# Kernel tuning notes

Measured on AMD Instinct MI355X. Metric: run time of the kernel, lower is better.

Reference implementation:

```python
import jax, jax.numpy as jnp
import numpy as np

GROUPS = 32
EPS = 1e-5


def _group_norm(x, scale, bias):
    B, C, H, W = x.shape
    xg = x.reshape(B, GROUPS, -1)
    mu = xg.mean(axis=-1, keepdims=True)
    var = jnp.mean(jnp.square(xg - mu), axis=-1, keepdims=True)
    xn = ((xg - mu) * jax.lax.rsqrt(var + EPS)).reshape(B, C, H, W)
    return xn * scale[None, :, None, None] + bias[None, :, None, None]


def _conv1x1(x, w, b):
    # x: [B,C,H,W], w: [O,C], b: [O]
    return jnp.einsum('bchw,oc->bohw', x, w) + b[None, :, None, None]


def setup_inputs() -> dict:
    key = jax.random.key(0)
    ks = jax.random.split(key, 6)
    B, C, H, W = 16, 512, 32, 32
    x = jax.random.normal(ks[0], (B, C, H, W), dtype=jnp.float32)
    # xavier_uniform for [C, C, 1, 1] conv: limit = sqrt(6 / (fan_in + fan_out)) = sqrt(6 / (2C))
    lim = float(np.sqrt(6.0 / (2 * C)))
    wq = jax.random.uniform(ks[1], (C, C), jnp.float32, -lim, lim)
    wk = jax.random.uniform(ks[2], (C, C), jnp.float32, -lim, lim)
    wv = jax.random.uniform(ks[3], (C, C), jnp.float32, -lim, lim)
    wo = jax.random.uniform(ks[4], (C, C), jnp.float32, -lim, lim) * 1e-5  # gain=1e-5
    zeros_c = jnp.zeros((C,), jnp.float32)
    return {
        'x': x,
        'gn_scale': jnp.ones((C,), jnp.float32),
        'gn_bias': zeros_c,
        'wq': wq, 'bq': zeros_c,
        'wk': wk, 'bk': zeros_c,
        'wv': wv, 'bv': zeros_c,
        'wo': wo, 'bo': zeros_c,
    }


def reference(x, gn_scale, gn_bias, wq, bq, wk, bk, wv, bv, wo, bo):
    B, C, H, W = x.shape
    N = H * W
    h = _group_norm(x, gn_scale, gn_bias)
    q = _conv1x1(h, wq, bq).reshape(B, C, N)  # [B,C,N]
    k = _conv1x1(h, wk, bk).reshape(B, C, N)
    v = _conv1x1(h, wv, bv).reshape(B, C, N)
    scale = 1.0 / jnp.sqrt(jnp.asarray(C, x.dtype))
    w = jnp.einsum('bcn,bcm->bnm', q, k) * scale  # [B,N,N]
    w = jax.nn.softmax(w, axis=-1)
    hv = jnp.einsum('bnm,bcm->bcn', w, v).reshape(B, C, H, W)
    out = _conv1x1(hv, wo, bo)
    return x + out
```

## Files before the change

kernel.cpp:

```cpp
#include <hip/hip_runtime.h>
#include <hip/hip_bf16.h>
#include <cstdint>

typedef unsigned char u8;
typedef float floatx4 __attribute__((ext_vector_type(4)));
typedef int intx8 __attribute__((ext_vector_type(8)));

__device__ __forceinline__ void gld_lds16(const void* g, void* l) {
    __builtin_amdgcn_global_load_lds(
        (const __attribute__((address_space(1))) unsigned int*)g,
        (__attribute__((address_space(3))) unsigned int*)l, 16, 0, 0);
}

__device__ __forceinline__ u8 f2fp8(float v) {
    return (u8)(__builtin_amdgcn_cvt_pk_fp8_f32(v, v, 0, false) & 0xff);
}
__device__ __forceinline__ unsigned int pack4_fp8(float a, float b, float c, float d) {
    unsigned int u = __builtin_amdgcn_cvt_pk_fp8_f32(a, b, 0, false);
    u = __builtin_amdgcn_cvt_pk_fp8_f32(c, d, u, true);
    return u;
}

__device__ __forceinline__ intx8 ld_frag(const u8* p, int lo, int hi) {
    uint4 a = *(const uint4*)(p + lo);
    uint4 b = *(const uint4*)(p + hi);
    intx8 r;
    r[0] = a.x; r[1] = a.y; r[2] = a.z; r[3] = a.w;
    r[4] = b.x; r[5] = b.y; r[6] = b.z; r[7] = b.w;
    return r;
}

__global__ __launch_bounds__(256) void setup_kernel(
    const float* __restrict__ x, const float* __restrict__ gs,
    const float* __restrict__ gb,
    const float* __restrict__ wq, const float* __restrict__ wk,
    const float* __restrict__ wv, const float* __restrict__ wo,
    const float* __restrict__ bq, const float* __restrict__ bk,
    const float* __restrict__ bv,
    u8* __restrict__ hT, u8* __restrict__ wqkv, u8* __restrict__ wob,
    float* __restrict__ bqkv, float* __restrict__ lsum)
{
    const int t = threadIdx.x;
    if (blockIdx.x >= 512) {
        int i = (blockIdx.x - 512) * 256 + t;
        if (i < 786432) {
            int which = i >> 18;
            int off = i & 262143;
            const float* src = which == 0 ? wq : which == 1 ? wk : wv;
            wqkv[i] = f2fp8(src[off]);
        } else {
            wob[i - 786432] = f2fp8(wo[i - 786432] * 262144.0f);
        }
        if (i < 1536)
            bqkv[i] = i < 512 ? bq[i] : (i < 1024 ? bk[i - 512] : bv[i - 1024]);
        if (i < 16384)
            lsum[i] = 0.0f;
        return;
    }
    const int b = blockIdx.x >> 5;
    const int g = blockIdx.x & 31;
    const int wave = t >> 6, lane = t & 63;
    const float4* x4 = (const float4*)(x + ((long long)b * 512 + g * 16) * 1024);

    float4 v[16];
    float s1 = 0.f, s2 = 0.f;
#pragma unroll
    for (int i = 0; i < 16; ++i) {
        v[i] = x4[i * 256 + t];
        s1 += v[i].x + v[i].y + v[i].z + v[i].w;
        s2 += v[i].x * v[i].x + v[i].y * v[i].y + v[i].z * v[i].z + v[i].w * v[i].w;
    }
#pragma unroll
    for (int m = 32; m; m >>= 1) {
        s1 += __shfl_xor(s1, m, 64);
        s2 += __shfl_xor(s2, m, 64);
    }
    __shared__ float red[2][4];
    __shared__ float stats[2];
    if (lane == 0) { red[0][wave] = s1; red[1][wave] = s2; }
    __syncthreads();
    if (t == 0) {
        float a = red[0][0] + red[0][1] + red[0][2] + red[0][3];
        float q = red[1][0] + red[1][1] + red[1][2] + red[1][3];
        float mu = a * (1.0f / 16384.0f);
        float var = q * (1.0f / 16384.0f) - mu * mu;
        stats[0] = mu;
        stats[1] = rsqrtf(var + 1e-5f);
    }
    __syncthreads();
    const float mu = stats[0], rs = stats[1];

#pragma unroll
    for (int i = 0; i < 16; ++i) {
        const float sc = gs[g * 16 + i] * rs;
        const float bi = gb[g * 16 + i] - mu * sc;
        v[i].x = v[i].x * sc + bi;
        v[i].y = v[i].y * sc + bi;
        v[i].z = v[i].z * sc + bi;
        v[i].w = v[i].w * sc + bi;
    }
    u8* hb = hT + (long long)b * 524288 + g * 16;
#pragma unroll
    for (int r = 0; r < 4; ++r) {
        uint4 o;
        o.x = pack4_fp8(v[0][r],  v[1][r],  v[2][r],  v[3][r]);
        o.y = pack4_fp8(v[4][r],  v[5][r],  v[6][r],  v[7][r]);
        o.z = pack4_fp8(v[8][r],  v[9][r],  v[10][r], v[11][r]);
        o.w = pack4_fp8(v[12][r], v[13][r], v[14][r], v[15][r]);
        *(uint4*)(hb + (long long)(4 * t + r) * 512) = o;
    }
}

template <int EPI>
__global__ __launch_bounds__(256, 3) void gemm_mx(
    const u8* __restrict__ A, long long sA,
    const u8* __restrict__ B, long long sB,
    void* __restrict__ C, long long sC,
    void* __restrict__ C2, void* __restrict__ C3,
    int ldC, int K,
    const float* __restrict__ bias,
    const float* __restrict__ resid, long long sR,
    float scale, float* __restrict__ lsum)
{
    __shared__ __align__(16) u8 smem[33792];
    const int tid = threadIdx.x;
    const int l = tid & 63;
    const int wave = tid >> 6;
    const int wm = wave >> 1, wn = wave & 1;
    const int bm = blockIdx.x, bn = blockIdx.y, b = blockIdx.z;

    const u8* Ab = A + (long long)b * sA + (long long)bm * 128 * K;
    const u8* Bb = B + (long long)b * sB + (long long)bn * 128 * K;

    const int srow = wave * 8 + (l >> 3);
    const int sg = ((l & 7) ^ ((l >> 3) & 7)) * 16;
    const u8* ga  = Ab + (long long)srow * K + sg;
    const u8* gbp = Bb + (long long)srow * K + sg;
    const long long c32 = (long long)32 * K;
    const int ldst = wave * 1024;

    const int q4 = l >> 4;
    const int glo = ((2 * q4) ^ (l & 7)) * 16;
    const int ghi = ((2 * q4 + 1) ^ (l & 7)) * 16;
    int arow[4], brow[4];
#pragma unroll
    for (int i = 0; i < 4; ++i) {
        arow[i] = (wm * 64 + i * 16 + (l & 15)) * 128;
        brow[i] = (wn * 64 + i * 16 + (l & 15)) * 128 + 16384;
    }

    floatx4 acc[4][4] = {};
    const int niter = K >> 7;

    for (int it = 0; it < niter; ++it) {
        const int k0 = it << 7;
#pragma unroll
        for (int c = 0; c < 4; ++c) {
            gld_lds16(ga + c * c32 + k0, smem + c * 4096 + ldst);
            gld_lds16(gbp + c * c32 + k0, smem + 16384 + c * 4096 + ldst);
        }
        __syncthreads();
        intx8 bfr[4];
#pragma unroll
        for (int j = 0; j < 4; ++j) bfr[j] = ld_frag(smem + brow[j], glo, ghi);
#pragma unroll
        for (int i = 0; i < 4; ++i) {
            intx8 af = ld_frag(smem + arow[i], glo, ghi);
#pragma unroll
            for (int j = 0; j < 4; ++j)
                acc[i][j] = __builtin_amdgcn_mfma_scale_f32_16x16x128_f8f6f4(
                    af, bfr[j], acc[i][j], 0, 0, 0, 127, 0, 127);
        }
        __syncthreads();
    }

    if (EPI == 3) {
        float* Cf = (float*)C;
#pragma unroll
        for (int i = 0; i < 4; ++i) {
            const int mrow = bm * 128 + wm * 64 + i * 16 + q4 * 4;
#pragma unroll
            for (int j = 0; j < 4; ++j) {
                const int ncol = bn * 128 + wn * 64 + j * 16 + (l & 15);
#pragma unroll
                for (int r = 0; r < 4; ++r) {
                    const int row = mrow + r;
                    float v = acc[i][j][r] * scale + bias[row] +
                              resid[(long long)b * sR + (long long)row * ldC + ncol];
                    Cf[(long long)b * sC + (long long)row * ldC + ncol] = v;
                }
            }
        }
    } else if (EPI == 1) {
        const int which = bn >> 2;
        u8* tile = smem;
#pragma unroll
        for (int i = 0; i < 4; ++i) {
            const int rl = wm * 64 + i * 16 + q4 * 4;
#pragma unroll
            for (int j = 0; j < 4; ++j) {
                const int cl = wn * 64 + j * 16 + (l & 15);
                const float badd = bias[bn * 128 + cl];
                if (which == 2) {
                    *(unsigned int*)(tile + cl * 144 + rl) =
                        pack4_fp8(acc[i][j][0] + badd, acc[i][j][1] + badd,
                                  acc[i][j][2] + badd, acc[i][j][3] + badd);
                } else {
#pragma unroll
                    for (int r = 0; r < 4; ++r)
                        tile[(rl + r) * 144 + cl] = f2fp8(acc[i][j][r] + badd);
                }
            }
        }
        __syncthreads();
        const int slot = (tid & 7) * 16;
#pragma unroll
        for (int p = 0; p < 4; ++p) {
            const int row = p * 32 + (tid >> 3);
            uint4 d = *(const uint4*)(tile + row * 144 + slot);
            u8* dst;
            if (which == 0)
                dst = (u8*)C + (long long)b * sC + (long long)(bm * 128 + row) * 512
                      + (bn & 3) * 128 + slot;
            else if (which == 1)
                dst = (u8*)C2 + (long long)b * sC + (long long)(bm * 128 + row) * 512
                      + (bn & 3) * 128 + slot;
            else
                dst = (u8*)C3 + (long long)b * sC + (long long)((bn & 3) * 128 + row) * 1024
                      + bm * 128 + slot;
            *(uint4*)dst = d;
        }
    } else if (EPI == 4) {
        u8* tile = smem;
#pragma unroll
        for (int i = 0; i < 4; ++i) {
            const int rl = wm * 64 + i * 16 + q4 * 4;
            float psum[4] = {0.f, 0.f, 0.f, 0.f};
#pragma unroll
            for (int j = 0; j < 4; ++j) {
                const int cl = wn * 64 + j * 16 + (l & 15);
#pragma unroll
                for (int r = 0; r < 4; ++r) {
                    float e = __expf(acc[i][j][r] * scale);
                    psum[r] += e;
                    tile[(rl + r) * 144 + cl] = f2fp8(e * 0.25f);
                }
            }
#pragma unroll
            for (int r = 0; r < 4; ++r) {
#pragma unroll
                for (int m = 8; m; m >>= 1) psum[r] += __shfl_xor(psum[r], m, 64);
            }
            if ((l & 15) == 0) {
                float* lp = lsum + b * 1024 + bm * 128 + rl;
#pragma unroll
                for (int r = 0; r < 4; ++r) atomicAdd(lp + r, psum[r]);
            }
        }
        __syncthreads();
        const int slot = (tid & 7) * 16;
#pragma unroll
        for (int p = 0; p < 4; ++p) {
            const int row = p * 32 + (tid >> 3);
            uint4 d = *(const uint4*)(tile + row * 144 + slot);
            u8* dst = (u8*)C + (long long)b * sC + (long long)(bm * 128 + row) * ldC
                      + bn * 128 + slot;
            *(uint4*)dst = d;
        }
    } else {
        u8* tile = smem;
#pragma unroll
        for (int i = 0; i < 4; ++i) {
            const int rl = wm * 64 + i * 16 + q4 * 4;
            const float* lp = lsum + b * 1024 + bm * 128 + rl;
            float rc[4];
#pragma unroll
            for (int r = 0; r < 4; ++r) rc[r] = 4.0f / lp[r];
#pragma unroll
            for (int j = 0; j < 4; ++j) {
                const int cl = wn * 64 + j * 16 + (l & 15);
#pragma unroll
                for (int r = 0; r < 4; ++r)
                    tile[(rl + r) * 144 + cl] = f2fp8(acc[i][j][r] * rc[r]);
            }
        }
        __syncthreads();
        const int slot = (tid & 7) * 16;
#pragma unroll
        for (int p = 0; p < 4; ++p) {
            const int row = p * 32 + (tid >> 3);
            uint4 d = *(const uint4*)(tile + row * 144 + slot);
            u8* dst = (u8*)C + (long long)b * sC + (long long)(bm * 128 + row) * ldC
                      + bn * 128 + slot;
            *(uint4*)dst = d;
        }
    }
}

extern "C" void kernel_launch(void* const* d_in, const int* in_sizes, int n_in,
                              void* d_out, int out_size, void* d_ws, size_t ws_size,
                              hipStream_t stream)
{
    const float* x  = (const float*)d_in[0];
    const float* gs = (const float*)d_in[1];
    const float* gb = (const float*)d_in[2];
    const float* wq = (const float*)d_in[3];
    const float* bq = (const float*)d_in[4];
    const float* wk = (const float*)d_in[5];
    const float* bk = (const float*)d_in[6];
    const float* wv = (const float*)d_in[7];
    const float* bv = (const float*)d_in[8];
    const float* wo = (const float*)d_in[9];
    const float* bo = (const float*)d_in[10];
    float* out = (float*)d_out;

    u8* p = (u8*)d_ws;
    u8* hT   = p; p += 8388608;
    u8* q    = p; p += 8388608;
    u8* k    = p; p += 8388608;
    u8* v    = p; p += 8388608;
    u8* wqkv = p; p += 786432;
    float* bqkv = (float*)p; p += 6144;
    u8* wob  = p; p += 262144;
    u8* P    = p; p += 16777216;
    u8* hvT  = p; p += 8388608;
    float* lsum = (float*)p; p += 65536;

    setup_kernel<<<4608, 256, 0, stream>>>(x, gs, gb, wq, wk, wv, wo, bq, bk, bv,
                                           hT, wqkv, wob, bqkv, lsum);

    gemm_mx<1><<<dim3(8, 12, 16), 256, 0, stream>>>(
        hT, 524288LL, wqkv, 0LL, q, 524288LL, k, v,
        512, 512, bqkv, nullptr, 0LL, 1.0f, nullptr);
    gemm_mx<4><<<dim3(8, 8, 16), 256, 0, stream>>>(
        q, 524288LL, k, 524288LL, P, 1048576LL, nullptr, nullptr,
        1024, 512, nullptr, nullptr, 0LL, 0.044194173824159216f, lsum);
    gemm_mx<5><<<dim3(8, 4, 16), 256, 0, stream>>>(
        P, 1048576LL, v, 524288LL, hvT, 524288LL, nullptr, nullptr,
        512, 1024, nullptr, nullptr, 0LL, 1.0f, lsum);
    gemm_mx<3><<<dim3(4, 8, 16), 256, 0, stream>>>(
        wob, 0LL, hvT, 524288LL, out, 524288LL, nullptr, nullptr,
        1024, 512, bo, x, 524288LL, 3.814697265625e-06f, nullptr);
}
```

Baseline: 177.8 us.

## Fuse QK^T, exp, and PV GEMMs into a single flash-style attention kernel

```diff
diff --git a/kernel.cpp b/kernel.cpp
--- a/kernel.cpp
+++ b/kernel.cpp
@@ -230,69 +230,141 @@
                       + bm * 128 + slot;
             *(uint4*)dst = d;
         }
-    } else if (EPI == 4) {
-        u8* tile = smem;
-#pragma unroll
-        for (int i = 0; i < 4; ++i) {
-            const int rl = wm * 64 + i * 16 + q4 * 4;
-            float psum[4] = {0.f, 0.f, 0.f, 0.f};
-#pragma unroll
-            for (int j = 0; j < 4; ++j) {
-                const int cl = wn * 64 + j * 16 + (l & 15);
-#pragma unroll
-                for (int r = 0; r < 4; ++r) {
-                    float e = __expf(acc[i][j][r] * scale);
-                    psum[r] += e;
-                    tile[(rl + r) * 144 + cl] = f2fp8(e * 0.25f);
-                }
+    }
+}
+
+__device__ __forceinline__ void stage_k_chunk(const u8* kb, u8* smem, int s,
+                                              int srow, int sg, int ldst) {
+    const int mt = s >> 2, kc = s & 3;
+    const u8* src = kb + (long long)(mt * 128 + srow) * 512 + kc * 128 + sg;
+    u8* dst = smem + (s & 1) * 16384 + ldst;
+#pragma unroll
+    for (int c = 0; c < 4; ++c)
+        gld_lds16(src + (long long)c * 16384, dst + c * 4096);
+}
+
+__global__ __launch_bounds__(256, 3) void attn_core(
+    const u8* __restrict__ qg, const u8* __restrict__ kg,
+    const u8* __restrict__ vg, u8* __restrict__ hvT)
+{
+    __shared__ __align__(16) u8 smem[53248];
+    const int tid = threadIdx.x;
+    const int l = tid & 63;
+    const int w = tid >> 6;
+    const int d = blockIdx.x;
+    const int b  = (d & 7) * 2 + ((d >> 8) & 1);
+    const int bq = (d >> 3) & 31;
+
+    const u8* qb = qg + (long long)b * 524288 + (long long)bq * 32 * 512;
+    const u8* kb = kg + (long long)b * 524288;
+    const u8* vb = vg + (long long)b * 524288;
+
+    const int srow = w * 8 + (l >> 3);
+    const int sg   = ((l & 7) ^ ((l >> 3) & 7)) * 16;
+    const int ldst = w * 1024;
+
+    const int q4 = l >> 4;
+    const int glo = ((2 * q4) ^ (l & 7)) * 16;
+    const int ghi = ((2 * q4 + 1) ^ (l & 7)) * 16;
+
+#pragma unroll
+    for (int kc = 0; kc < 4; ++kc)
+        gld_lds16(qb + (long long)srow * 512 + kc * 128 + sg,
+                  smem + 32768 + kc * 4096 + ldst);
+    stage_k_chunk(kb, smem, 0, srow, sg, ldst);
+    __syncthreads();
+
+    floatx4 acc_pv[8][2] = {};
+    float psum[2] = {0.f, 0.f};
+    const float scale = 0.044194173824159216f;
+    u8* E = smem + 49152;
+
+    for (int mt = 0; mt < 16; ++mt) {
+        floatx4 acc_s[2][2] = {};
+#pragma unroll
+        for (int kc = 0; kc < 4; ++kc) {
+            const int s = mt * 4 + kc;
+            if (s + 1 < 64) stage_k_chunk(kb, smem, s + 1, srow, sg, ldst);
+            const u8* kbuf = smem + (s & 1) * 16384;
+            const u8* qbuf = smem + 32768 + kc * 4096;
+            intx8 qf[2];
+#pragma unroll
+            for (int j = 0; j < 2; ++j)
+                qf[j] = ld_frag(qbuf + (j * 16 + (l & 15)) * 128, glo, ghi);
+#pragma unroll
+            for (int i = 0; i < 2; ++i) {
+                intx8 kf = ld_frag(kbuf + (w * 32 + i * 16 + (l & 15)) * 128, glo, ghi);
+#pragma unroll
+                for (int j = 0; j < 2; ++j)
+                    acc_s[i][j] = __builtin_amdgcn_mfma_scale_f32_16x16x128_f8f6f4(
+                        kf, qf[j], acc_s[i][j], 0, 0, 0, 127, 0, 127);
             }
-#pragma unroll
-            for (int r = 0; r < 4; ++r) {
-#pragma unroll
-                for (int m = 8; m; m >>= 1) psum[r] += __shfl_xor(psum[r], m, 64);
+            __syncthreads();
+        }
+#pragma unroll
+        for (int i = 0; i < 2; ++i) {
+#pragma unroll
+            for (int j = 0; j < 2; ++j) {
+                float e0 = __expf(acc_s[i][j][0] * scale);
+                float e1 = __expf(acc_s[i][j][1] * scale);
+                float e2 = __expf(acc_s[i][j][2] * scale);
+                float e3 = __expf(acc_s[i][j][3] * scale);
+                psum[j] += e0 + e1 + e2 + e3;
+                const int n = j * 16 + (l & 15);
+                const int m0 = w * 32 + i * 16 + q4 * 4;
+                *(unsigned int*)(E + n * 128 + (m0 ^ ((n & 7) * 16))) =
+                    pack4_fp8(e0 * 0.25f, e1 * 0.25f, e2 * 0.25f, e3 * 0.25f);
             }
-            if ((l & 15) == 0) {
-                float* lp = lsum + b * 1024 + bm * 128 + rl;
-#pragma unroll
-                for (int r = 0; r < 4; ++r) atomicAdd(lp + r, psum[r]);
-            }
         }
         __syncthreads();
-        const int slot = (tid & 7) * 16;
-#pragma unroll
-        for (int p = 0; p < 4; ++p) {
-            const int row = p * 32 + (tid >> 3);
-            uint4 d = *(const uint4*)(tile + row * 144 + slot);
-            u8* dst = (u8*)C + (long long)b * sC + (long long)(bm * 128 + row) * ldC
-                      + bn * 128 + slot;
-            *(uint4*)dst = d;
-        }
-    } else {
-        u8* tile = smem;
-#pragma unroll
-        for (int i = 0; i < 4; ++i) {
-            const int rl = wm * 64 + i * 16 + q4 * 4;
-            const float* lp = lsum + b * 1024 + bm * 128 + rl;
-            float rc[4];
-#pragma unroll
-            for (int r = 0; r < 4; ++r) rc[r] = 4.0f / lp[r];
-#pragma unroll
-            for (int j = 0; j < 4; ++j) {
-                const int cl = wn * 64 + j * 16 + (l & 15);
-#pragma unroll
-                for (int r = 0; r < 4; ++r)
-                    tile[(rl + r) * 144 + cl] = f2fp8(acc[i][j][r] * rc[r]);
-            }
+        intx8 ef[2];
+#pragma unroll
+        for (int j = 0; j < 2; ++j)
+            ef[j] = ld_frag(E + (j * 16 + (l & 15)) * 128, glo, ghi);
+        const u8* vrow = vb + (long long)(w * 128 + (l & 15)) * 1024 + mt * 128 + q4 * 32;
+#pragma unroll
+        for (int i = 0; i < 8; ++i) {
+            const u8* vp = vrow + (long long)i * 16 * 1024;
+            uint4 a = *(const uint4*)(vp);
+            uint4 bb = *(const uint4*)(vp + 16);
+            intx8 vf;
+            vf[0] = a.x;  vf[1] = a.y;  vf[2] = a.z;  vf[3] = a.w;
+            vf[4] = bb.x; vf[5] = bb.y; vf[6] = bb.z; vf[7] = bb.w;
+#pragma unroll
+            for (int j = 0; j < 2; ++j)
+                acc_pv[i][j] = __builtin_amdgcn_mfma_scale_f32_16x16x128_f8f6f4(
+                    vf, ef[j], acc_pv[i][j], 0, 0, 0, 127, 0, 127);
         }
         __syncthreads();
-        const int slot = (tid & 7) * 16;
-#pragma unroll
-        for (int p = 0; p < 4; ++p) {
-            const int row = p * 32 + (tid >> 3);
-            uint4 d = *(const uint4*)(tile + row * 144 + slot);
-            u8* dst = (u8*)C + (long long)b * sC + (long long)(bm * 128 + row) * ldC
-                      + bn * 128 + slot;
-            *(uint4*)dst = d;
+    }
+
+#pragma unroll
+    for (int j = 0; j < 2; ++j) {
+        psum[j] += __shfl_xor(psum[j], 16, 64);
+        psum[j] += __shfl_xor(psum[j], 32, 64);
+    }
+    float* sb = (float*)(smem + 49152);
+    if (l < 16) {
+        sb[w * 32 + l]      = psum[0];
+        sb[w * 32 + 16 + l] = psum[1];
+    }
+    __syncthreads();
+    float rln[2];
+#pragma unroll
+    for (int j = 0; j < 2; ++j) {
+        const int n = j * 16 + (l & 15);
+        rln[j] = 4.0f / (sb[n] + sb[32 + n] + sb[64 + n] + sb[96 + n]);
+    }
+    u8* ob = hvT + (long long)b * 524288 + (long long)(bq * 32) * 512;
+#pragma unroll
+    for (int i = 0; i < 8; ++i) {
+#pragma unroll
+        for (int j = 0; j < 2; ++j) {
+            const int n = j * 16 + (l & 15);
+            const int c = w * 128 + i * 16 + q4 * 4;
+            *(unsigned int*)(ob + (long long)n * 512 + c) =
+                pack4_fp8(acc_pv[i][j][0] * rln[j], acc_pv[i][j][1] * rln[j],
+                          acc_pv[i][j][2] * rln[j], acc_pv[i][j][3] * rln[j]);
         }
     }
 }
@@ -325,6 +397,7 @@
     u8* P    = p; p += 16777216;
     u8* hvT  = p; p += 8388608;
     float* lsum = (float*)p; p += 65536;
+    (void)P;
 
     setup_kernel<<<4608, 256, 0, stream>>>(x, gs, gb, wq, wk, wv, wo, bq, bk, bv,
                                            hT, wqkv, wob, bqkv, lsum);
@@ -332,12 +405,9 @@
     gemm_mx<1><<<dim3(8, 12, 16), 256, 0, stream>>>(
         hT, 524288LL, wqkv, 0LL, q, 524288LL, k, v,
         512, 512, bqkv, nullptr, 0LL, 1.0f, nullptr);
-    gemm_mx<4><<<dim3(8, 8, 16), 256, 0, stream>>>(
-        q, 524288LL, k, 524288LL, P, 1048576LL, nullptr, nullptr,
-        1024, 512, nullptr, nullptr, 0LL, 0.044194173824159216f, lsum);
-    gemm_mx<5><<<dim3(8, 4, 16), 256, 0, stream>>>(
-        P, 1048576LL, v, 524288LL, hvT, 524288LL, nullptr, nullptr,
-        512, 1024, nullptr, nullptr, 0LL, 1.0f, lsum);
+
+    attn_core<<<dim3(512, 1, 1), 256, 0, stream>>>(q, k, v, hvT);
+
     gemm_mx<3><<<dim3(4, 8, 16), 256, 0, stream>>>(
         wob, 0LL, hvT, 524288LL, out, 524288LL, nullptr, nullptr,
         1024, 512, bo, x, 524288LL, 3.814697265625e-06f, nullptr);
```

Measured after the change: 235.8 us. 32.7% more time.
